# Kernel optimization log

Hardware: AMD Instinct MI355X
Metric: run time of the kernel (lower is better)

Reference implementation:

```python
import jax, jax.numpy as jnp
import numpy as np

SVDPROB = 0.8


def _usvt(x, mask):
    # x: [B, C, H, W] in [0,1]; mask: [B, H, C*W] {0,1}
    B, C, H, W = x.shape
    img = x * 2.0 - 1.0
    # channel-concat along width: [B, H, C*W] (ch0 | ch1 | ch2)
    img2d = jnp.transpose(img, (0, 2, 1, 3)).reshape(B, H, C * W)
    m = mask.astype(img2d.dtype)
    p_obs = jnp.mean(m, axis=(1, 2))  # fraction of observed entries per image
    # SVD of masked matrix; min(H, C*W) == H, so full_matrices=False keeps all
    # singular triplets that the original dense reconstruction uses.
    u, s, vt = jnp.linalg.svd(img2d * m, full_matrices=False)  # u:[B,H,H], s:[B,H], vt:[B,H,CW]
    k = int(SVDPROB * H)  # number of retained singular values
    s_trunc = jnp.where(jnp.arange(H) < k, s, jnp.zeros_like(s))
    # rank-k reconstruction, scaled by 1/p_obs
    Wrec = jnp.einsum('bhr,br,brw->bhw', u, s_trunc, vt) / p_obs[:, None, None]
    est = (jnp.clip(Wrec, -1.0, 1.0) + 1.0) / 2.0  # [B, H, C*W]
    # split channels back (valid because H == W in the original indexing)
    out = jnp.transpose(est.reshape(B, H, C, W), (0, 2, 1, 3))
    return out


def setup_inputs() -> dict:
    key = jax.random.key(0)
    k1, k2 = jax.random.split(key)
    B, C, H, W = 64, 3, 224, 224
    x = jax.random.uniform(k1, (B, C, H, W), dtype=jnp.float32)
    mask = jax.random.randint(k2, (B, H, C * W), 0, 2, dtype=jnp.int32)
    return {"x": x, "mask": mask}


def reference(x, mask):
    # UVSTModule.forward with module = identity
    return _usvt(x, mask)
```

## Files before the change

kernel.cpp:

```cpp
#include <hip/hip_runtime.h>

#define BATCH 64
#define NH 224
#define NCW 672
#define CSTRIDE 256
#define KKEEP 179
#define NTAIL 45
#define NSWEEPS 8
#define EPS2 1e-18f

__device__ __forceinline__ float fast_rcp(float x) { return __builtin_amdgcn_rcpf(x); }
__device__ __forceinline__ float fast_rsq(float x) { return __builtin_amdgcn_rsqf(x); }
__device__ __forceinline__ float fast_sqrt(float x) { return __builtin_amdgcn_sqrtf(x); }

__device__ __forceinline__ float wave_sum(float s) {
    s += __shfl_xor(s, 32); s += __shfl_xor(s, 16); s += __shfl_xor(s, 8);
    s += __shfl_xor(s, 4);  s += __shfl_xor(s, 2);  s += __shfl_xor(s, 1);
    return s;
}

__device__ __forceinline__ float dpp_sum_bcast(float x) {
    int t;
    t = __builtin_amdgcn_update_dpp(0, __float_as_int(x), 0x111, 0xF, 0xF, true);
    x += __int_as_float(t);
    t = __builtin_amdgcn_update_dpp(0, __float_as_int(x), 0x112, 0xF, 0xF, true);
    x += __int_as_float(t);
    t = __builtin_amdgcn_update_dpp(0, __float_as_int(x), 0x114, 0xF, 0xF, true);
    x += __int_as_float(t);
    t = __builtin_amdgcn_update_dpp(0, __float_as_int(x), 0x118, 0xF, 0xF, true);
    x += __int_as_float(t);
    t = __builtin_amdgcn_update_dpp(0, __float_as_int(x), 0x142, 0xA, 0xF, true);
    x += __int_as_float(t);
    t = __builtin_amdgcn_update_dpp(0, __float_as_int(x), 0x143, 0xC, 0xF, true);
    x += __int_as_float(t);
    return __int_as_float(__builtin_amdgcn_readlane(__float_as_int(x), 63));
}

__device__ __forceinline__ float dot4(const float4& A, const float4& B) {
    return A.x * B.x + A.y * B.y + A.z * B.z + A.w * B.w;
}

#define ROTA(A, B, LA, LB, APQ) do {                                          \
    float _apq = (APQ);                                                       \
    float _tau = (LB - LA) * 0.5f * fast_rcp(_apq);                           \
    float _t = copysignf(fast_rcp(fabsf(_tau) + fast_sqrt(1.f + _tau * _tau)), _tau); \
    _t = (_apq * _apq > EPS2 * LA * LB) ? _t : 0.f;                           \
    float _cc = fast_rsq(1.f + _t * _t);                                      \
    float _ss = _t * _cc;                                                     \
    float _ax = A.x, _ay = A.y, _az = A.z, _aw = A.w;                         \
    A.x = _cc * _ax - _ss * B.x; B.x = _ss * _ax + _cc * B.x;                 \
    A.y = _cc * _ay - _ss * B.y; B.y = _ss * _ay + _cc * B.y;                 \
    A.z = _cc * _az - _ss * B.z; B.z = _ss * _az + _cc * B.z;                 \
    A.w = _cc * _aw - _ss * B.w; B.w = _ss * _aw + _cc * B.w;                 \
    LA -= _t * _apq; LB += _t * _apq;                                         \
} while (0)

__global__ __launch_bounds__(256) void pobs_kernel(const int* __restrict__ mask,
                                                   float* __restrict__ invp) {
    int b = blockIdx.x, tid = threadIdx.x;
    const int* mb = mask + (size_t)b * NH * NCW;
    int s = 0;
    for (int i = tid; i < NH * NCW; i += 256) s += mb[i];
    __shared__ int red[256];
    red[tid] = s;
    __syncthreads();
    for (int o = 128; o; o >>= 1) {
        if (tid < o) red[tid] += red[tid + o];
        __syncthreads();
    }
    if (tid == 0) invp[b] = (float)(NH * NCW) / (float)red[0];
}

__global__ void pad_kernel(float* __restrict__ G) {
    int idx = blockIdx.x * 256 + threadIdx.x;
    int b = idx / (NH * 32);
    int rem = idx - b * (NH * 32);
    int j = rem >> 5;
    int i = NH + (rem & 31);
    G[((size_t)b * NH + j) * CSTRIDE + i] = 0.f;
}

__global__ __launch_bounds__(256) void gram_kernel(const float* __restrict__ x,
                                                   const int* __restrict__ mask,
                                                   float* __restrict__ G) {
    int b = blockIdx.y;
    int tile = blockIdx.x;
    int ti = 0, tt = tile;
    while (tt >= 7 - ti) { tt -= 7 - ti; ++ti; }
    int tj = ti + tt;
    int i0 = ti * 32, j0 = tj * 32;
    __shared__ float As[32][33];
    __shared__ float Bs[32][33];
    int tid = threadIdx.x;
    int tx = tid & 31;
    int ty = tid >> 5;
    float acc0 = 0, acc1 = 0, acc2 = 0, acc3 = 0;
    const float* xb = x + (size_t)b * 3 * NH * NH;
    const int* mb = mask + (size_t)b * NH * NCW;
    for (int ks = 0; ks < 21; ++ks) {
        int k0 = ks * 32;
        int c = k0 / NH;
        int w0 = k0 - c * NH;
        __syncthreads();
        for (int l = tid; l < 1024; l += 256) {
            int dk = l & 31, di = l >> 5;
            int hA = i0 + di, hB = j0 + di;
            float xa = xb[(c * NH + hA) * NH + w0 + dk];
            float xc = xb[(c * NH + hB) * NH + w0 + dk];
            As[di][dk] = mb[hA * NCW + k0 + dk] ? 2.f * xa - 1.f : 0.f;
            Bs[di][dk] = mb[hB * NCW + k0 + dk] ? 2.f * xc - 1.f : 0.f;
        }
        __syncthreads();
#pragma unroll
        for (int kk = 0; kk < 32; ++kk) {
            float bv = Bs[tx][kk];
            acc0 += As[ty][kk] * bv;
            acc1 += As[ty + 8][kk] * bv;
            acc2 += As[ty + 16][kk] * bv;
            acc3 += As[ty + 24][kk] * bv;
        }
    }
    float* Gb = G + (size_t)b * NH * CSTRIDE;
    int j = j0 + tx;
    int i = i0 + ty;
    Gb[j * CSTRIDE + i] = acc0;
    Gb[j * CSTRIDE + i + 8] = acc1;
    Gb[j * CSTRIDE + i + 16] = acc2;
    Gb[j * CSTRIDE + i + 24] = acc3;
    if (ti != tj) {
        Gb[i * CSTRIDE + j] = acc0;
        Gb[(i + 8) * CSTRIDE + j] = acc1;
        Gb[(i + 16) * CSTRIDE + j] = acc2;
        Gb[(i + 24) * CSTRIDE + j] = acc3;
    }
}

__global__ __launch_bounds__(1024) void colnorm_kernel(const float* __restrict__ G,
                                                       float* __restrict__ lam) {
    int b = blockIdx.x;
    const float* Gb = G + (size_t)b * NH * CSTRIDE;
    int tid = threadIdx.x, lane = tid & 63, wid = tid >> 6;
    for (int k = 0; k < 14; ++k) {
        int j = wid * 14 + k;
        float4 v = ((const float4*)(Gb + j * CSTRIDE))[lane];
        float d = wave_sum(v.x * v.x + v.y * v.y + v.z * v.z + v.w * v.w);
        if (lane == 0) lam[b * NH + j] = d;
    }
}

__device__ __forceinline__ void cross49(float4* cp, float* lp, float4* cq, float* lq) {
#pragma unroll
    for (int r7 = 0; r7 < 7; ++r7) {
        float part[7], red[7];
#pragma unroll
        for (int i = 0; i < 7; ++i) part[i] = dot4(cp[i], cq[(i + r7) % 7]);
#pragma unroll
        for (int i = 0; i < 7; ++i) red[i] = dpp_sum_bcast(part[i]);
#pragma unroll
        for (int i = 0; i < 7; ++i) {
            const int j = (i + r7) % 7;
            ROTA(cp[i], cq[j], lp[i], lq[j], red[i]);
        }
    }
}

__device__ __forceinline__ void pair_round(float* __restrict__ Gb,
                                           float* __restrict__ sLam,
                                           int bp, int bq, int lane, bool intra) {
    int cp0 = bp * 7, cq0 = bq * 7;
    float4 c[14];
    float l[14];
#pragma unroll
    for (int k = 0; k < 7; ++k) {
        c[k]     = ((const float4*)(Gb + (cp0 + k) * CSTRIDE))[lane];
        c[7 + k] = ((const float4*)(Gb + (cq0 + k) * CSTRIDE))[lane];
        l[k]     = sLam[cp0 + k];
        l[7 + k] = sLam[cq0 + k];
    }
    if (intra) {
#pragma unroll
        for (int r7 = 0; r7 < 7; ++r7) {
            float part[6], red[6];
#pragma unroll
            for (int k = 1; k <= 3; ++k) {
                const int a = (r7 + k) % 7, d = (r7 + 7 - k) % 7;
                part[k - 1] = dot4(c[a], c[d]);
                part[k + 2] = dot4(c[7 + a], c[7 + d]);
            }
#pragma unroll
            for (int k = 0; k < 6; ++k) red[k] = dpp_sum_bcast(part[k]);
#pragma unroll
            for (int k = 1; k <= 3; ++k) {
                const int a = (r7 + k) % 7, d = (r7 + 7 - k) % 7;
                ROTA(c[a], c[d], l[a], l[d], red[k - 1]);
                ROTA(c[7 + a], c[7 + d], l[7 + a], l[7 + d], red[k + 2]);
            }
        }
    }
    cross49(c, l, c + 7, l + 7);
#pragma unroll
    for (int k = 0; k < 7; ++k) {
        ((float4*)(Gb + (cp0 + k) * CSTRIDE))[lane] = c[k];
        ((float4*)(Gb + (cq0 + k) * CSTRIDE))[lane] = c[7 + k];
        if (lane == 0) {
            sLam[cp0 + k] = l[k];
            sLam[cq0 + k] = l[7 + k];
        }
    }
}

__global__ __launch_bounds__(256, 1) void jacobi_meet_kernel(float* __restrict__ G,
                                                             float* __restrict__ lam,
                                                             int mr, int do_intra) {
    int b = blockIdx.y;
    int m = blockIdx.x;
    int ga, gb;
    if (m == 0) { ga = 7; gb = mr; }
    else        { ga = (mr + m) % 7; gb = (mr + 7 - m) % 7; }
    float* Gb = G + (size_t)b * NH * CSTRIDE;
    float* lamg = lam + b * NH;
    __shared__ float sLam[NH];
    int tid = threadIdx.x, lane = tid & 63, w = tid >> 6;

    if (tid < 28) sLam[ga * 28 + tid] = lamg[ga * 28 + tid];
    else if (tid < 56) sLam[gb * 28 + (tid - 28)] = lamg[gb * 28 + (tid - 28)];
    __syncthreads();

    if (do_intra) {
        int g = (w < 2) ? ga : gb;
        int wi = w & 1;
        for (int rr = 0; rr < 3; ++rr) {
            int lp, lq;
            if (wi == 0) { lp = 3; lq = rr; }
            else { lp = (rr + 1) % 3; lq = (rr + 2) % 3; }
            pair_round(Gb, sLam, g * 4 + lp, g * 4 + lq, lane, rr == 0);
            __syncthreads();
        }
    }

    int bp = ga * 4 + w;
    float4 cp[7];
    float lp[7];
#pragma unroll
    for (int k = 0; k < 7; ++k) {
        cp[k] = ((const float4*)(Gb + (bp * 7 + k) * CSTRIDE))[lane];
        lp[k] = sLam[bp * 7 + k];
    }
    for (int rr = 0; rr < 4; ++rr) {
        int bq = gb * 4 + ((w + rr) & 3);
        float4 cq[7];
        float lq[7];
#pragma unroll
        for (int k = 0; k < 7; ++k) {
            cq[k] = ((const float4*)(Gb + (bq * 7 + k) * CSTRIDE))[lane];
            lq[k] = sLam[bq * 7 + k];
        }
        cross49(cp, lp, cq, lq);
#pragma unroll
        for (int k = 0; k < 7; ++k) {
            ((float4*)(Gb + (bq * 7 + k) * CSTRIDE))[lane] = cq[k];
            if (lane == 0) sLam[bq * 7 + k] = lq[k];
        }
        __syncthreads();
    }
#pragma unroll
    for (int k = 0; k < 7; ++k) {
        ((float4*)(Gb + (bp * 7 + k) * CSTRIDE))[lane] = cp[k];
        if (lane == 0) sLam[bp * 7 + k] = lp[k];
    }
    __syncthreads();

    if (tid < 28) lamg[ga * 28 + tid] = sLam[ga * 28 + tid];
    else if (tid < 56) lamg[gb * 28 + (tid - 28)] = sLam[gb * 28 + (tid - 28)];
}

__global__ __launch_bounds__(256) void select_kernel(const float* __restrict__ G,
                                                     int* __restrict__ tail_idx,
                                                     float* __restrict__ invl2) {
    int b = blockIdx.x;
    const float* Gb = G + (size_t)b * NH * CSTRIDE;
    __shared__ float lam[NH];
    __shared__ int cnt;
    int tid = threadIdx.x, lane = tid & 63, wid = tid >> 6;
    if (tid == 0) cnt = 0;
    for (int j = wid * 56; j < wid * 56 + 56; ++j) {
        float4 v = ((const float4*)(Gb + j * CSTRIDE))[lane];
        float d = wave_sum(v.x * v.x + v.y * v.y + v.z * v.z + v.w * v.w);
        if (lane == 0) lam[j] = d;
    }
    __syncthreads();
    if (tid < NH) {
        float my = lam[tid];
        int rank = 0;
        for (int i = 0; i < NH; ++i) {
            float o = lam[i];
            rank += (o > my) ? 1 : ((o == my && i < tid) ? 1 : 0);
        }
        if (rank >= KKEEP) {
            int pos = atomicAdd(&cnt, 1);
            tail_idx[b * NTAIL + pos] = tid;
            invl2[b * NTAIL + pos] = 1.f / my;
        }
    }
}

__global__ __launch_bounds__(128) void ctail_kernel(const float* __restrict__ G,
                                                    const float* __restrict__ x,
                                                    const int* __restrict__ mask,
                                                    const int* __restrict__ tail_idx,
                                                    const float* __restrict__ invl2,
                                                    float* __restrict__ C) {
    int b = blockIdx.y;
    int wchunk = blockIdx.x;
    __shared__ float sT[NH * 48];
    __shared__ float sInv[NTAIL];
    __shared__ int sIdx[NTAIL];
    int tid = threadIdx.x;
    if (tid < NTAIL) {
        sIdx[tid] = tail_idx[b * NTAIL + tid];
        sInv[tid] = invl2[b * NTAIL + tid];
    }
    __syncthreads();
    for (int idx = tid; idx < NTAIL * NH; idx += 128) {
        int t = idx / NH, h = idx - t * NH;
        sT[h * 48 + t] = G[((size_t)b * NH + sIdx[t]) * CSTRIDE + h];
    }
    for (int idx = tid; idx < NH * 3; idx += 128) {
        int h = idx / 3, t = NTAIL + idx - h * 3;
        sT[h * 48 + t] = 0.f;
    }
    __syncthreads();
    if (tid < 112) {
        int wp = wchunk * 112 + tid;
        int c = wp / NH;
        int w = wp - c * NH;
        const float* xb = x + ((size_t)(b * 3 + c) * NH) * NH + w;
        const int* mb = mask + (size_t)b * NH * NCW + wp;
        float acc[48];
#pragma unroll
        for (int t = 0; t < 48; ++t) acc[t] = 0.f;
        for (int h = 0; h < NH; h += 4) {
            float a0 = mb[(h + 0) * NCW] ? 2.f * xb[(h + 0) * NH] - 1.f : 0.f;
            float a1 = mb[(h + 1) * NCW] ? 2.f * xb[(h + 1) * NH] - 1.f : 0.f;
            float a2 = mb[(h + 2) * NCW] ? 2.f * xb[(h + 2) * NH] - 1.f : 0.f;
            float a3 = mb[(h + 3) * NCW] ? 2.f * xb[(h + 3) * NH] - 1.f : 0.f;
            const float4* r0 = (const float4*)(sT + (h + 0) * 48);
            const float4* r1 = (const float4*)(sT + (h + 1) * 48);
            const float4* r2 = (const float4*)(sT + (h + 2) * 48);
            const float4* r3 = (const float4*)(sT + (h + 3) * 48);
#pragma unroll
            for (int t4 = 0; t4 < 12; ++t4) {
                float4 s0 = r0[t4], s1 = r1[t4], s2 = r2[t4], s3 = r3[t4];
                acc[4 * t4 + 0] += s0.x * a0 + s1.x * a1 + s2.x * a2 + s3.x * a3;
                acc[4 * t4 + 1] += s0.y * a0 + s1.y * a1 + s2.y * a2 + s3.y * a3;
                acc[4 * t4 + 2] += s0.z * a0 + s1.z * a1 + s2.z * a2 + s3.z * a3;
                acc[4 * t4 + 3] += s0.w * a0 + s1.w * a1 + s2.w * a2 + s3.w * a3;
            }
        }
        float* Cb = C + ((size_t)b * NTAIL) * NCW + wp;
#pragma unroll
        for (int t = 0; t < NTAIL; ++t) Cb[t * NCW] = acc[t] * sInv[t];
    }
}

__global__ __launch_bounds__(256) void out_kernel(const float* __restrict__ G,
                                                  const float* __restrict__ x,
                                                  const int* __restrict__ mask,
                                                  const int* __restrict__ tail_idx,
                                                  const float* __restrict__ C,
                                                  const float* __restrict__ invp,
                                                  float* __restrict__ out) {
    int b = blockIdx.z, hc = blockIdx.y, wc = blockIdx.x;
    int h0 = hc * 32, w0 = wc * 96;
    __shared__ float sCol[NTAIL * 32];
    __shared__ float sC[NTAIL * 96];
    __shared__ int sIdx[NTAIL];
    int tid = threadIdx.x;
    if (tid < NTAIL) sIdx[tid] = tail_idx[b * NTAIL + tid];
    __syncthreads();
    for (int i = tid; i < NTAIL * 32; i += 256) {
        int t = i >> 5, hl = i & 31;
        sCol[i] = G[((size_t)b * NH + sIdx[t]) * CSTRIDE + h0 + hl];
    }
    for (int i = tid; i < NTAIL * 96; i += 256) {
        int t = i / 96, wl = i - t * 96;
        sC[i] = C[((size_t)b * NTAIL + t) * NCW + w0 + wl];
    }
    __syncthreads();
    float ip = invp[b];
    for (int i = tid; i < 32 * 96; i += 256) {
        int hl = i / 96, wl = i - hl * 96;
        int h = h0 + hl, wp = w0 + wl;
        int c = wp / NH, w = wp - c * NH;
        float a = mask[(size_t)b * NH * NCW + h * NCW + wp]
                      ? 2.f * x[((size_t)(b * 3 + c) * NH + h) * NH + w] - 1.f
                      : 0.f;
        float corr = 0.f;
#pragma unroll
        for (int t = 0; t < NTAIL; ++t) corr += sCol[t * 32 + hl] * sC[t * 96 + wl];
        float val = (a - corr) * ip;
        val = fminf(1.f, fmaxf(-1.f, val));
        out[((size_t)(b * 3 + c) * NH + h) * NH + w] = (val + 1.f) * 0.5f;
    }
}

extern "C" void kernel_launch(void* const* d_in, const int* in_sizes, int n_in,
                              void* d_out, int out_size, void* d_ws, size_t ws_size,
                              hipStream_t stream) {
    const float* x = (const float*)d_in[0];
    const int* mask = (const int*)d_in[1];
    float* out = (float*)d_out;
    char* ws = (char*)d_ws;

    const size_t off_G = 0;
    const size_t sz_G = (size_t)BATCH * NH * CSTRIDE * 4;
    const size_t off_invp = off_G + sz_G;
    const size_t off_tail = off_invp + 256;
    const size_t off_invl2 = off_tail + (size_t)BATCH * NTAIL * 4;
    const size_t off_C = off_invl2 + (size_t)BATCH * NTAIL * 4;
    const size_t sz_C = (size_t)BATCH * NTAIL * NCW * 4;
    const size_t off_lam = off_C + sz_C;

    float* G = (float*)(ws + off_G);
    float* invp = (float*)(ws + off_invp);
    int* tail = (int*)(ws + off_tail);
    float* invl2 = (float*)(ws + off_invl2);
    float* C = (float*)(ws + off_C);
    float* lam = (float*)(ws + off_lam);

    pobs_kernel<<<BATCH, 256, 0, stream>>>(mask, invp);
    pad_kernel<<<(BATCH * NH * 32) / 256, 256, 0, stream>>>(G);
    gram_kernel<<<dim3(28, BATCH), 256, 0, stream>>>(x, mask, G);
    colnorm_kernel<<<BATCH, 1024, 0, stream>>>(G, lam);
    for (int sweep = 0; sweep < NSWEEPS; ++sweep)
        for (int mr = 0; mr < 7; ++mr)
            jacobi_meet_kernel<<<dim3(4, BATCH), 256, 0, stream>>>(G, lam, mr, mr == 0);
    select_kernel<<<BATCH, 256, 0, stream>>>(G, tail, invl2);
    ctail_kernel<<<dim3(6, BATCH), 128, 0, stream>>>(G, x, mask, tail, invl2, C);
    out_kernel<<<dim3(7, 7, BATCH), 256, 0, stream>>>(G, x, mask, tail, C, invp, out);
}
```

Baseline: 2.370 ms.

## Split tail projection over height chunks and cut Jacobi sweeps to seven

The ctail kernel now splits the 224-row reduction into four 56-row chunks, giving four times as many blocks. Each chunk writes a partial C buffer, and out_kernel sums the four partials and applies the inverse eigenvalue scaling when it loads them. The shared tile stride becomes 52 to reduce bank conflicts. Jacobi sweeps drop from 8 to 7, removing seven kernel launches of work at some risk to eigen-decomposition accuracy.

Result: faster. 2.052 ms (-13.4%).

```diff
diff --git a/kernel.cpp b/kernel.cpp
--- a/kernel.cpp
+++ b/kernel.cpp
@@ -6,8 +6,9 @@
 #define CSTRIDE 256
 #define KKEEP 179
 #define NTAIL 45
-#define NSWEEPS 8
+#define NSWEEPS 7
 #define EPS2 1e-18f
+#define STP 52
 
 __device__ __forceinline__ float fast_rcp(float x) { return __builtin_amdgcn_rcpf(x); }
 __device__ __forceinline__ float fast_rsq(float x) { return __builtin_amdgcn_rsqf(x); }
@@ -308,26 +309,23 @@
                                                     const float* __restrict__ x,
                                                     const int* __restrict__ mask,
                                                     const int* __restrict__ tail_idx,
-                                                    const float* __restrict__ invl2,
-                                                    float* __restrict__ C) {
-    int b = blockIdx.y;
+                                                    float* __restrict__ Cp) {
+    int b = blockIdx.z;
+    int hchunk = blockIdx.y;
     int wchunk = blockIdx.x;
-    __shared__ float sT[NH * 48];
-    __shared__ float sInv[NTAIL];
+    int h0 = hchunk * 56;
+    __shared__ float sT[56 * STP];
     __shared__ int sIdx[NTAIL];
     int tid = threadIdx.x;
-    if (tid < NTAIL) {
-        sIdx[tid] = tail_idx[b * NTAIL + tid];
-        sInv[tid] = invl2[b * NTAIL + tid];
-    }
-    __syncthreads();
-    for (int idx = tid; idx < NTAIL * NH; idx += 128) {
-        int t = idx / NH, h = idx - t * NH;
-        sT[h * 48 + t] = G[((size_t)b * NH + sIdx[t]) * CSTRIDE + h];
-    }
-    for (int idx = tid; idx < NH * 3; idx += 128) {
-        int h = idx / 3, t = NTAIL + idx - h * 3;
-        sT[h * 48 + t] = 0.f;
+    if (tid < NTAIL) sIdx[tid] = tail_idx[b * NTAIL + tid];
+    __syncthreads();
+    for (int idx = tid; idx < NTAIL * 56; idx += 128) {
+        int t = idx / 56, hh = idx - t * 56;
+        sT[hh * STP + t] = G[((size_t)b * NH + sIdx[t]) * CSTRIDE + h0 + hh];
+    }
+    for (int idx = tid; idx < 56 * (STP - NTAIL); idx += 128) {
+        int hh = idx / (STP - NTAIL), t = NTAIL + idx - hh * (STP - NTAIL);
+        sT[hh * STP + t] = 0.f;
     }
     __syncthreads();
     if (tid < 112) {
@@ -339,15 +337,16 @@
         float acc[48];
 #pragma unroll
         for (int t = 0; t < 48; ++t) acc[t] = 0.f;
-        for (int h = 0; h < NH; h += 4) {
+        for (int hh = 0; hh < 56; hh += 4) {
+            int h = h0 + hh;
             float a0 = mb[(h + 0) * NCW] ? 2.f * xb[(h + 0) * NH] - 1.f : 0.f;
             float a1 = mb[(h + 1) * NCW] ? 2.f * xb[(h + 1) * NH] - 1.f : 0.f;
             float a2 = mb[(h + 2) * NCW] ? 2.f * xb[(h + 2) * NH] - 1.f : 0.f;
             float a3 = mb[(h + 3) * NCW] ? 2.f * xb[(h + 3) * NH] - 1.f : 0.f;
-            const float4* r0 = (const float4*)(sT + (h + 0) * 48);
-            const float4* r1 = (const float4*)(sT + (h + 1) * 48);
-            const float4* r2 = (const float4*)(sT + (h + 2) * 48);
-            const float4* r3 = (const float4*)(sT + (h + 3) * 48);
+            const float4* r0 = (const float4*)(sT + (hh + 0) * STP);
+            const float4* r1 = (const float4*)(sT + (hh + 1) * STP);
+            const float4* r2 = (const float4*)(sT + (hh + 2) * STP);
+            const float4* r3 = (const float4*)(sT + (hh + 3) * STP);
 #pragma unroll
             for (int t4 = 0; t4 < 12; ++t4) {
                 float4 s0 = r0[t4], s1 = r1[t4], s2 = r2[t4], s3 = r3[t4];
@@ -357,9 +356,9 @@
                 acc[4 * t4 + 3] += s0.w * a0 + s1.w * a1 + s2.w * a2 + s3.w * a3;
             }
         }
-        float* Cb = C + ((size_t)b * NTAIL) * NCW + wp;
-#pragma unroll
-        for (int t = 0; t < NTAIL; ++t) Cb[t * NCW] = acc[t] * sInv[t];
+        float* Cb = Cp + ((size_t)hchunk * BATCH + b) * (size_t)NTAIL * NCW + wp;
+#pragma unroll
+        for (int t = 0; t < NTAIL; ++t) Cb[t * NCW] = acc[t];
     }
 }
 
@@ -367,16 +366,22 @@
                                                   const float* __restrict__ x,
                                                   const int* __restrict__ mask,
                                                   const int* __restrict__ tail_idx,
-                                                  const float* __restrict__ C,
+                                                  const float* __restrict__ Cp,
+                                                  const float* __restrict__ invl2,
                                                   const float* __restrict__ invp,
                                                   float* __restrict__ out) {
     int b = blockIdx.z, hc = blockIdx.y, wc = blockIdx.x;
     int h0 = hc * 32, w0 = wc * 96;
+    const size_t PS = (size_t)BATCH * NTAIL * NCW;
     __shared__ float sCol[NTAIL * 32];
     __shared__ float sC[NTAIL * 96];
+    __shared__ float sInv[NTAIL];
     __shared__ int sIdx[NTAIL];
     int tid = threadIdx.x;
-    if (tid < NTAIL) sIdx[tid] = tail_idx[b * NTAIL + tid];
+    if (tid < NTAIL) {
+        sIdx[tid] = tail_idx[b * NTAIL + tid];
+        sInv[tid] = invl2[b * NTAIL + tid];
+    }
     __syncthreads();
     for (int i = tid; i < NTAIL * 32; i += 256) {
         int t = i >> 5, hl = i & 31;
@@ -384,7 +389,9 @@
     }
     for (int i = tid; i < NTAIL * 96; i += 256) {
         int t = i / 96, wl = i - t * 96;
-        sC[i] = C[((size_t)b * NTAIL + t) * NCW + w0 + wl];
+        size_t base = ((size_t)b * NTAIL + t) * NCW + w0 + wl;
+        float s = Cp[base] + Cp[base + PS] + Cp[base + 2 * PS] + Cp[base + 3 * PS];
+        sC[i] = s * sInv[t];
     }
     __syncthreads();
     float ip = invp[b];
@@ -417,16 +424,15 @@
     const size_t off_invp = off_G + sz_G;
     const size_t off_tail = off_invp + 256;
     const size_t off_invl2 = off_tail + (size_t)BATCH * NTAIL * 4;
-    const size_t off_C = off_invl2 + (size_t)BATCH * NTAIL * 4;
-    const size_t sz_C = (size_t)BATCH * NTAIL * NCW * 4;
-    const size_t off_lam = off_C + sz_C;
+    const size_t off_lam = off_invl2 + (size_t)BATCH * NTAIL * 4;
+    const size_t off_Cp = off_lam + (size_t)BATCH * NH * 4;
 
     float* G = (float*)(ws + off_G);
     float* invp = (float*)(ws + off_invp);
     int* tail = (int*)(ws + off_tail);
     float* invl2 = (float*)(ws + off_invl2);
-    float* C = (float*)(ws + off_C);
     float* lam = (float*)(ws + off_lam);
+    float* Cp = (float*)(ws + off_Cp);
 
     pobs_kernel<<<BATCH, 256, 0, stream>>>(mask, invp);
     pad_kernel<<<(BATCH * NH * 32) / 256, 256, 0, stream>>>(G);
@@ -436,6 +442,6 @@
         for (int mr = 0; mr < 7; ++mr)
             jacobi_meet_kernel<<<dim3(4, BATCH), 256, 0, stream>>>(G, lam, mr, mr == 0);
     select_kernel<<<BATCH, 256, 0, stream>>>(G, tail, invl2);
-    ctail_kernel<<<dim3(6, BATCH), 128, 0, stream>>>(G, x, mask, tail, invl2, C);
-    out_kernel<<<dim3(7, 7, BATCH), 256, 0, stream>>>(G, x, mask, tail, C, invp, out);
-}
+    ctail_kernel<<<dim3(6, 4, BATCH), 128, 0, stream>>>(G, x, mask, tail, Cp);
+    out_kernel<<<dim3(7, 7, BATCH), 256, 0, stream>>>(G, x, mask, tail, Cp, invl2, invp, out);
+}
```
